# Kernel optimization log

Hardware: AMD Instinct MI355X
Metric: run time of the kernel (lower is better)

Reference implementation:

```python
import jax, jax.numpy as jnp
import numpy as np

EPS = 1e-08
LAMBDA_SIM = 1.0
LAMBDA_SPARSITY = 0.001
B, D, K = 8192, 4096, 64


def setup_inputs() -> dict:
    key = jax.random.key(0)
    k1, k2, k3, k4, k5 = jax.random.split(key, 5)
    labels = jax.random.randint(k1, (B,), 0, K)
    hard_class_probs = jax.nn.one_hot(labels, K, dtype=jnp.float32)  # [B,K] hard one-hot
    return {
        "hard_class_probs": hard_class_probs,
        "masked_activations_1b": jax.random.normal(k2, (B, D), dtype=jnp.float32),
        "masked_activations_8b": jax.random.normal(k3, (B, D), dtype=jnp.float32),
        "mask_1b": jax.random.uniform(k4, (B, D), dtype=jnp.float32),
        "mask_8b": jax.random.uniform(k5, (B, D), dtype=jnp.float32),
    }


def _classwise_pairwise_cossim(acts, hard_class_probs):
    # F.normalize(p=2, dim=-1, eps=EPS): x / max(||x||, eps)
    norms = jnp.sqrt(jnp.sum(acts * acts, axis=-1, keepdims=True))
    norm_acts = acts / jnp.maximum(norms, EPS)                      # [B,D]
    S = norm_acts @ norm_acts.T                                      # [B,B] gram of unit vectors
    diag = jnp.sum(norm_acts * norm_acts, axis=-1)                   # [B] (== diag(S))
    M = (hard_class_probs > 0.5).astype(acts.dtype)                  # [B,K] hard membership
    n = jnp.sum(M, axis=0)                                           # [K] class counts
    SM = S @ M                                                       # [B,K]
    mSm = jnp.sum(M * SM, axis=0)                                    # [K] sum_{i,j in class} S_ij
    sum_diag = M.T @ diag                                            # [K]
    pair_sum = 0.5 * (mSm - sum_diag)                                # sum over i<j pairs
    n_pairs = 0.5 * n * (n - 1.0)
    valid = n >= 2.0
    per_class_mean = jnp.where(valid, pair_sum / jnp.maximum(n_pairs, 1.0), 0.0)
    n_valid = jnp.sum(valid.astype(acts.dtype))
    return jnp.where(n_valid > 0, jnp.sum(per_class_mean) / jnp.maximum(n_valid, 1.0), 0.0)


def _binary_entropy(p):
    p = jnp.clip(p, EPS, 1.0 - EPS)
    return jnp.mean(-(p * jnp.log(p) + (1.0 - p) * jnp.log(1.0 - p)))


def _combined_loss(hard_class_probs, masked_activations, mask):
    sim_loss = -_classwise_pairwise_cossim(masked_activations, hard_class_probs)
    sparsity_loss = _binary_entropy(mask)
    total = LAMBDA_SIM * sim_loss + LAMBDA_SPARSITY * sparsity_loss
    return total, sim_loss, sparsity_loss


def reference(hard_class_probs, masked_activations_1b, masked_activations_8b, mask_1b, mask_8b):
    loss_1b, sim_1b, sp_1b = _combined_loss(hard_class_probs, masked_activations_1b, mask_1b)
    loss_8b, sim_8b, sp_8b = _combined_loss(hard_class_probs, masked_activations_8b, mask_8b)
    total_loss = loss_1b + loss_8b
    return (total_loss, sim_1b, sim_8b, sp_1b, sp_8b)
```

## Files before the change

kernel.cpp:

```cpp
#include <hip/hip_runtime.h>
#include <math.h>

#define B_ 8192
#define D_ 4096
#define K_ 64
#define EPSF 1e-8f
#define LN2F 0.69314718056f
#define ENT_GRID 2048
#define SPLITS 16

typedef float f32x4 __attribute__((ext_vector_type(4)));


__global__ void k_init(int* __restrict__ z) {
  if (threadIdx.x < 192) z[threadIdx.x] = 0;
}

__global__ void k_labels(const float* __restrict__ probs, int* __restrict__ labels,
                         int* __restrict__ counts, int* __restrict__ rowlist) {
  int row = blockIdx.x * 4 + (threadIdx.x >> 6);
  int lane = threadIdx.x & 63;
  float p = probs[(size_t)row * K_ + lane];
  unsigned long long m = __ballot(p > 0.5f);
  if (lane == 0) {
    int k = __ffsll(m) - 1;
    if (k >= 0) {
      labels[row] = k;
      int pos = atomicAdd(&counts[k], 1);
      rowlist[k * B_ + pos] = row;
    }
  }
}

__global__ __launch_bounds__(256) void k_classnorm(
    const float* __restrict__ a1, const float* __restrict__ a8,
    const int* __restrict__ counts, const int* __restrict__ rowlist,
    const int* __restrict__ labels, float* __restrict__ Cpart1, float* __restrict__ Cpart8,
    float* __restrict__ sd1, float* __restrict__ sd8) {
  int bid = blockIdx.x;
  const float* a = (bid < 256) ? a1 : a8;
  float* Cpart = (bid < 256) ? Cpart1 : Cpart8;
  float* sd = (bid < 256) ? sd1 : sd8;
  bid &= 255;
  int k = bid & 63;
  int blkSplit = bid >> 6;
  int wave = threadIdx.x >> 6;
  int lane = threadIdx.x & 63;
  int split = blkSplit * 4 + wave;
  int cnt = counts[k];
  int beg = (cnt * split) / SPLITS;
  int end = (cnt * (split + 1)) / SPLITS;
  const int* rl = rowlist + k * B_;

  f32x4 acc[16];
#pragma unroll
  for (int j = 0; j < 16; ++j) acc[j] = 0.f;

  for (int r = beg; r < end; ++r) {
    int row = rl[r];
    const f32x4* rp = (const f32x4*)(a + (size_t)row * D_);
    f32x4 v[16];
#pragma unroll
    for (int j = 0; j < 16; ++j) v[j] = rp[lane + 64 * j];
    float s = 0.f;
#pragma unroll
    for (int j = 0; j < 16; ++j)
      s += v[j].x * v[j].x + v[j].y * v[j].y + v[j].z * v[j].z + v[j].w * v[j].w;
#pragma unroll
    for (int o = 32; o > 0; o >>= 1) s += __shfl_xor(s, o);
    float w = 1.0f / fmaxf(sqrtf(s), EPSF);
#pragma unroll
    for (int j = 0; j < 16; ++j) acc[j] += w * v[j];
    if (lane == 0) atomicAdd(&sd[labels[row]], s * w * w);
  }

  float* cp = Cpart + ((size_t)split * K_ + k) * D_;
#pragma unroll
  for (int j = 0; j < 16; ++j) *(f32x4*)(cp + 4 * (lane + 64 * j)) = acc[j];
}

__global__ __launch_bounds__(256) void k_msm(const float* __restrict__ Cpart1,
                                             const float* __restrict__ Cpart8,
                                             float* __restrict__ msp1,
                                             float* __restrict__ msp8) {
  __shared__ float lds[4];
  int b = blockIdx.x;
  const float* Cpart = (b < 256) ? Cpart1 : Cpart8;
  float* msp = (b < 256) ? msp1 : msp8;
  b &= 255;
  int k = b >> 2;
  int q = b & 3;
  int t = threadIdx.x;
  int col = q * 1024 + 4 * t;
  f32x4 c = 0.f;
#pragma unroll
  for (int s = 0; s < SPLITS; ++s)
    c += *(const f32x4*)(Cpart + ((size_t)s * K_ + k) * D_ + col);
  float sq = c.x * c.x + c.y * c.y + c.z * c.z + c.w * c.w;
#pragma unroll
  for (int o = 32; o > 0; o >>= 1) sq += __shfl_down(sq, o);
  if ((t & 63) == 0) lds[t >> 6] = sq;
  __syncthreads();
  if (t == 0) msp[blockIdx.x & 255] = lds[0] + lds[1] + lds[2] + lds[3];
}

__device__ __forceinline__ float ent1(float p) {
  p = fminf(fmaxf(p, EPSF), 1.0f - EPSF);
  float q = 1.0f - p;
  float lp = __builtin_amdgcn_logf(p);
  float lq = __builtin_amdgcn_logf(fmaxf(q, 1e-38f));
  return -(p * lp + q * lq);
}

__device__ __forceinline__ float ent4(f32x4 v) {
  return ent1(v.x) + ent1(v.y) + ent1(v.z) + ent1(v.w);
}

__global__ __launch_bounds__(256) void k_entropy(const f32x4* __restrict__ m1,
                                                 const f32x4* __restrict__ m8,
                                                 double* __restrict__ entpart) {
  __shared__ float lds[8];
  const int CHUNK = (B_ * D_ / 4) / ENT_GRID;
  int base = blockIdx.x * CHUNK;
  int t = threadIdx.x;
  float s1 = 0.f, s8 = 0.f;
#pragma unroll
  for (int o = 0; o < 4; ++o) {
    f32x4 a[4], b[4];
#pragma unroll
    for (int j = 0; j < 4; ++j) {
      int idx = base + t + (o * 4 + j) * 256;
      a[j] = m1[idx];
      b[j] = m8[idx];
    }
#pragma unroll
    for (int j = 0; j < 4; ++j) {
      s1 += ent4(a[j]);
      s8 += ent4(b[j]);
    }
  }
#pragma unroll
  for (int o = 32; o > 0; o >>= 1) {
    s1 += __shfl_down(s1, o);
    s8 += __shfl_down(s8, o);
  }
  int wid = t >> 6;
  if ((t & 63) == 0) { lds[wid] = s1; lds[4 + wid] = s8; }
  __syncthreads();
  if (t == 0) {
    float t1 = lds[0] + lds[1] + lds[2] + lds[3];
    float t8 = lds[4] + lds[5] + lds[6] + lds[7];
    entpart[blockIdx.x]            = (double)(t1 * LN2F);
    entpart[ENT_GRID + blockIdx.x] = (double)(t8 * LN2F);
  }
}

__global__ void k_final(const double* __restrict__ entpart, const int* __restrict__ counts,
                        const float* __restrict__ sd1, const float* __restrict__ sd8,
                        const float* __restrict__ msp1, const float* __restrict__ msp8,
                        float* __restrict__ out) {
  __shared__ double dl[8];
  int t = threadIdx.x;
  double e1 = 0.0, e8 = 0.0;
  for (int i = t; i < ENT_GRID; i += 256) {
    e1 += entpart[i];
    e8 += entpart[ENT_GRID + i];
  }
#pragma unroll
  for (int o = 32; o > 0; o >>= 1) {
    e1 += __shfl_down(e1, o);
    e8 += __shfl_down(e8, o);
  }
  int wid = t >> 6;
  if ((t & 63) == 0) { dl[wid] = e1; dl[4 + wid] = e8; }
  __syncthreads();
  float pcm1 = 0.f, pcm8 = 0.f, valid = 0.f;
  if (t < K_) {
    float mSm1 = msp1[t * 4] + msp1[t * 4 + 1] + msp1[t * 4 + 2] + msp1[t * 4 + 3];
    float mSm8 = msp8[t * 4] + msp8[t * 4 + 1] + msp8[t * 4 + 2] + msp8[t * 4 + 3];
    float n = (float)counts[t];
    bool v = (n >= 2.0f);
    float np = fmaxf(0.5f * n * (n - 1.0f), 1.0f);
    valid = v ? 1.0f : 0.f;
    pcm1 = v ? 0.5f * (mSm1 - sd1[t]) / np : 0.f;
    pcm8 = v ? 0.5f * (mSm8 - sd8[t]) / np : 0.f;
  }
#pragma unroll
  for (int o = 32; o > 0; o >>= 1) {
    pcm1 += __shfl_down(pcm1, o);
    pcm8 += __shfl_down(pcm8, o);
    valid += __shfl_down(valid, o);
  }
  if (t == 0) {
    double etot1 = dl[0] + dl[1] + dl[2] + dl[3];
    double etot8 = dl[4] + dl[5] + dl[6] + dl[7];
    float sp1 = (float)(etot1 / (double)((long long)B_ * D_));
    float sp8 = (float)(etot8 / (double)((long long)B_ * D_));
    float cs1 = (valid > 0.f) ? pcm1 / fmaxf(valid, 1.0f) : 0.f;
    float cs8 = (valid > 0.f) ? pcm8 / fmaxf(valid, 1.0f) : 0.f;
    float sim1 = -cs1, sim8 = -cs8;
    out[0] = sim1 + sim8 + 0.001f * (sp1 + sp8);
    out[1] = sim1;
    out[2] = sim8;
    out[3] = sp1;
    out[4] = sp8;
  }
}


extern "C" void kernel_launch(void* const* d_in, const int* in_sizes, int n_in,
                              void* d_out, int out_size, void* d_ws, size_t ws_size,
                              hipStream_t stream) {
  const float* probs = (const float*)d_in[0];
  const float* a1 = (const float*)d_in[1];
  const float* a8 = (const float*)d_in[2];
  const float* m1 = (const float*)d_in[3];
  const float* m8 = (const float*)d_in[4];
  float* out = (float*)d_out;
  char* ws = (char*)d_ws;

  double* entpart = (double*)(ws + 0);
  int* labels = (int*)(ws + 32768);
  int* counts = (int*)(ws + 65536);
  float* sd1 = (float*)(ws + 65792);
  float* sd8 = (float*)(ws + 66048);
  float* msp1 = (float*)(ws + 66304);
  float* msp8 = (float*)(ws + 67328);
  int* rowlist = (int*)(ws + 69632);
  float* Cpart1 = (float*)(ws + 2166784);
  float* Cpart8 = (float*)(ws + 18944000);

  k_init<<<1, 256, 0, stream>>>(counts);
  k_labels<<<B_ / 4, 256, 0, stream>>>(probs, labels, counts, rowlist);
  k_classnorm<<<512, 256, 0, stream>>>(a1, a8, counts, rowlist, labels, Cpart1, Cpart8, sd1,
                                       sd8);
  k_entropy<<<ENT_GRID, 256, 0, stream>>>((const f32x4*)m1, (const f32x4*)m8, entpart);
  k_msm<<<512, 256, 0, stream>>>(Cpart1, Cpart8, msp1, msp8);
  k_final<<<1, 256, 0, stream>>>(entpart, counts, sd1, sd8, msp1, msp8, out);
}
```

Baseline: 183.6 us.

## Split each activation row across four waves with LDS norm reduction

The class-norm kernel now has one block per (class, split), and its four waves each cover a quarter of a row's columns instead of each wave handling whole rows. The squared norm is combined across waves through a double-buffered shared-memory array with a block barrier on every row. This cuts the per-wave register footprint from sixteen vector accumulators to four, quadruples the block count to fill more of the GPU, and drops the labels lookup for the atomic. The cost is a __syncthreads per row and a smaller per-wave memory footprint in flight.

```diff
diff --git a/kernel.cpp b/kernel.cpp
--- a/kernel.cpp
+++ b/kernel.cpp
@@ -35,48 +35,55 @@
 __global__ __launch_bounds__(256) void k_classnorm(
     const float* __restrict__ a1, const float* __restrict__ a8,
     const int* __restrict__ counts, const int* __restrict__ rowlist,
-    const int* __restrict__ labels, float* __restrict__ Cpart1, float* __restrict__ Cpart8,
-    float* __restrict__ sd1, float* __restrict__ sd8) {
+    float* __restrict__ Cpart1, float* __restrict__ Cpart8, float* __restrict__ sd1,
+    float* __restrict__ sd8) {
+  __shared__ float lred[2][4];
   int bid = blockIdx.x;
-  const float* a = (bid < 256) ? a1 : a8;
-  float* Cpart = (bid < 256) ? Cpart1 : Cpart8;
-  float* sd = (bid < 256) ? sd1 : sd8;
-  bid &= 255;
+  const int NBLK = K_ * SPLITS;
+  const float* a = (bid < NBLK) ? a1 : a8;
+  float* Cpart = (bid < NBLK) ? Cpart1 : Cpart8;
+  float* sd = (bid < NBLK) ? sd1 : sd8;
+  bid = (bid < NBLK) ? bid : bid - NBLK;
   int k = bid & 63;
-  int blkSplit = bid >> 6;
+  int split = bid >> 6;
   int wave = threadIdx.x >> 6;
   int lane = threadIdx.x & 63;
-  int split = blkSplit * 4 + wave;
   int cnt = counts[k];
   int beg = (cnt * split) / SPLITS;
   int end = (cnt * (split + 1)) / SPLITS;
   const int* rl = rowlist + k * B_;
 
-  f32x4 acc[16];
-#pragma unroll
-  for (int j = 0; j < 16; ++j) acc[j] = 0.f;
-
-  for (int r = beg; r < end; ++r) {
+  f32x4 acc0 = 0.f, acc1 = 0.f, acc2 = 0.f, acc3 = 0.f;
+  int par = 0;
+  for (int r = beg; r < end; ++r, par ^= 1) {
     int row = rl[r];
-    const f32x4* rp = (const f32x4*)(a + (size_t)row * D_);
-    f32x4 v[16];
-#pragma unroll
-    for (int j = 0; j < 16; ++j) v[j] = rp[lane + 64 * j];
-    float s = 0.f;
-#pragma unroll
-    for (int j = 0; j < 16; ++j)
-      s += v[j].x * v[j].x + v[j].y * v[j].y + v[j].z * v[j].z + v[j].w * v[j].w;
+    const f32x4* rp = (const f32x4*)(a + (size_t)row * D_) + (wave * 256 + lane);
+    f32x4 v0 = rp[0];
+    f32x4 v1 = rp[64];
+    f32x4 v2 = rp[128];
+    f32x4 v3 = rp[192];
+    float s = v0.x * v0.x + v0.y * v0.y + v0.z * v0.z + v0.w * v0.w;
+    s += v1.x * v1.x + v1.y * v1.y + v1.z * v1.z + v1.w * v1.w;
+    s += v2.x * v2.x + v2.y * v2.y + v2.z * v2.z + v2.w * v2.w;
+    s += v3.x * v3.x + v3.y * v3.y + v3.z * v3.z + v3.w * v3.w;
 #pragma unroll
     for (int o = 32; o > 0; o >>= 1) s += __shfl_xor(s, o);
-    float w = 1.0f / fmaxf(sqrtf(s), EPSF);
-#pragma unroll
-    for (int j = 0; j < 16; ++j) acc[j] += w * v[j];
-    if (lane == 0) atomicAdd(&sd[labels[row]], s * w * w);
-  }
-
-  float* cp = Cpart + ((size_t)split * K_ + k) * D_;
-#pragma unroll
-  for (int j = 0; j < 16; ++j) *(f32x4*)(cp + 4 * (lane + 64 * j)) = acc[j];
+    if (lane == 0) lred[par][wave] = s;
+    __syncthreads();
+    float stot = lred[par][0] + lred[par][1] + lred[par][2] + lred[par][3];
+    float w = 1.0f / fmaxf(sqrtf(stot), EPSF);
+    acc0 += w * v0;
+    acc1 += w * v1;
+    acc2 += w * v2;
+    acc3 += w * v3;
+    if (threadIdx.x == 0) atomicAdd(&sd[k], stot * w * w);
+  }
+
+  float* cp = Cpart + ((size_t)split * K_ + k) * D_ + wave * 1024;
+  *(f32x4*)(cp + 4 * lane) = acc0;
+  *(f32x4*)(cp + 4 * (64 + lane)) = acc1;
+  *(f32x4*)(cp + 4 * (128 + lane)) = acc2;
+  *(f32x4*)(cp + 4 * (192 + lane)) = acc3;
 }
 
 __global__ __launch_bounds__(256) void k_msm(const float* __restrict__ Cpart1,
@@ -232,8 +239,8 @@
 
   k_init<<<1, 256, 0, stream>>>(counts);
   k_labels<<<B_ / 4, 256, 0, stream>>>(probs, labels, counts, rowlist);
-  k_classnorm<<<512, 256, 0, stream>>>(a1, a8, counts, rowlist, labels, Cpart1, Cpart8, sd1,
-                                       sd8);
+  k_classnorm<<<2 * K_ * SPLITS, 256, 0, stream>>>(a1, a8, counts, rowlist, Cpart1, Cpart8,
+                                                   sd1, sd8);
   k_entropy<<<ENT_GRID, 256, 0, stream>>>((const f32x4*)m1, (const f32x4*)m8, entpart);
   k_msm<<<512, 256, 0, stream>>>(Cpart1, Cpart8, msp1, msp8);
   k_final<<<1, 256, 0, stream>>>(entpart, counts, sd1, sd8, msp1, msp8, out);
```

New measurement: 193.1 us. 5.1% more time.

## Fuse class-norm and entropy passes into a persistent work-stealing kernel

Applied to the files above, without the earlier changes.

Merges the class-sum and binary-entropy kernels into one persistent kernel whose waves take interleaved tasks from an atomic counter, so both memory-bound streams run at once and load balance across the GPU. Row loads in the class-sum path are double-buffered to overlap memory with compute. Splits per class double to 32, which needs a larger Cpart workspace and gives k_msm twice as many partials to reduce. The per-row sd atomic becomes one per-task atomic, and the labels array is dropped. The cost is a global atomic per task and higher register pressure from the two 16-vector buffers.

```diff
diff --git a/kernel.cpp b/kernel.cpp
--- a/kernel.cpp
+++ b/kernel.cpp
@@ -7,17 +7,17 @@
 #define EPSF 1e-8f
 #define LN2F 0.69314718056f
 #define ENT_GRID 2048
-#define SPLITS 16
+#define SPLITS 32
+#define GTASKS 4096
+#define TTASKS 8192
 
 typedef float f32x4 __attribute__((ext_vector_type(4)));
 
 
-__global__ void k_init(int* __restrict__ z) {
-  if (threadIdx.x < 192) z[threadIdx.x] = 0;
-}
-
-__global__ void k_labels(const float* __restrict__ probs, int* __restrict__ labels,
-                         int* __restrict__ counts, int* __restrict__ rowlist) {
+__global__ void k_init(int* __restrict__ z) { z[threadIdx.x] = 0; }
+
+__global__ void k_labels(const float* __restrict__ probs, int* __restrict__ counts,
+                         int* __restrict__ rowlist) {
   int row = blockIdx.x * 4 + (threadIdx.x >> 6);
   int lane = threadIdx.x & 63;
   float p = probs[(size_t)row * K_ + lane];
@@ -25,58 +25,100 @@
   if (lane == 0) {
     int k = __ffsll(m) - 1;
     if (k >= 0) {
-      labels[row] = k;
       int pos = atomicAdd(&counts[k], 1);
       rowlist[k * B_ + pos] = row;
     }
   }
 }
 
-__global__ __launch_bounds__(256) void k_classnorm(
+__device__ __forceinline__ float ent1(float p) {
+  p = fminf(fmaxf(p, EPSF), 1.0f - EPSF);
+  float q = 1.0f - p;
+  float lp = __builtin_amdgcn_logf(p);
+  float lq = __builtin_amdgcn_logf(fmaxf(q, 1e-38f));
+  return -(p * lp + q * lq);
+}
+
+__device__ __forceinline__ float ent4(f32x4 v) {
+  return ent1(v.x) + ent1(v.y) + ent1(v.z) + ent1(v.w);
+}
+
+#define MLOADROW(V, ROW)                                                        \
+  {                                                                             \
+    const f32x4* rp_ = (const f32x4*)(a + (size_t)(ROW)*D_) + lane;             \
+    _Pragma("unroll") for (int j = 0; j < 16; ++j) V[j] = rp_[64 * j];          \
+  }
+
+#define MCONSUME(V)                                                             \
+  {                                                                             \
+    float s_ = 0.f;                                                             \
+    _Pragma("unroll") for (int j = 0; j < 16; ++j) s_ +=                        \
+        V[j].x * V[j].x + V[j].y * V[j].y + V[j].z * V[j].z + V[j].w * V[j].w;  \
+    _Pragma("unroll") for (int o = 32; o > 0; o >>= 1) s_ += __shfl_xor(s_, o); \
+    float w_ = 1.0f / fmaxf(sqrtf(s_), EPSF);                                   \
+    _Pragma("unroll") for (int j = 0; j < 16; ++j) acc[j] += w_ * V[j];         \
+    sdacc += s_ * w_ * w_;                                                      \
+  }
+
+__global__ __launch_bounds__(256) void k_mega(
     const float* __restrict__ a1, const float* __restrict__ a8,
+    const f32x4* __restrict__ m1, const f32x4* __restrict__ m8,
     const int* __restrict__ counts, const int* __restrict__ rowlist,
-    const int* __restrict__ labels, float* __restrict__ Cpart1, float* __restrict__ Cpart8,
-    float* __restrict__ sd1, float* __restrict__ sd8) {
-  int bid = blockIdx.x;
-  const float* a = (bid < 256) ? a1 : a8;
-  float* Cpart = (bid < 256) ? Cpart1 : Cpart8;
-  float* sd = (bid < 256) ? sd1 : sd8;
-  bid &= 255;
-  int k = bid & 63;
-  int blkSplit = bid >> 6;
-  int wave = threadIdx.x >> 6;
+    float* __restrict__ Cpart1, float* __restrict__ Cpart8, float* __restrict__ sd1,
+    float* __restrict__ sd8, double* __restrict__ entpart, int* __restrict__ ctr) {
   int lane = threadIdx.x & 63;
-  int split = blkSplit * 4 + wave;
-  int cnt = counts[k];
-  int beg = (cnt * split) / SPLITS;
-  int end = (cnt * (split + 1)) / SPLITS;
-  const int* rl = rowlist + k * B_;
-
-  f32x4 acc[16];
-#pragma unroll
-  for (int j = 0; j < 16; ++j) acc[j] = 0.f;
-
-  for (int r = beg; r < end; ++r) {
-    int row = rl[r];
-    const f32x4* rp = (const f32x4*)(a + (size_t)row * D_);
-    f32x4 v[16];
-#pragma unroll
-    for (int j = 0; j < 16; ++j) v[j] = rp[lane + 64 * j];
-    float s = 0.f;
-#pragma unroll
-    for (int j = 0; j < 16; ++j)
-      s += v[j].x * v[j].x + v[j].y * v[j].y + v[j].z * v[j].z + v[j].w * v[j].w;
-#pragma unroll
-    for (int o = 32; o > 0; o >>= 1) s += __shfl_xor(s, o);
-    float w = 1.0f / fmaxf(sqrtf(s), EPSF);
-#pragma unroll
-    for (int j = 0; j < 16; ++j) acc[j] += w * v[j];
-    if (lane == 0) atomicAdd(&sd[labels[row]], s * w * w);
-  }
-
-  float* cp = Cpart + ((size_t)split * K_ + k) * D_;
-#pragma unroll
-  for (int j = 0; j < 16; ++j) *(f32x4*)(cp + 4 * (lane + 64 * j)) = acc[j];
+  for (;;) {
+    int task = 0;
+    if (lane == 0) task = atomicAdd(ctr, 1);
+    task = __shfl(task, 0);
+    if (task >= TTASKS) break;
+    int id = task >> 1;
+    if (task & 1) {
+      const f32x4* base = ((id >> 11) ? m8 : m1) + (size_t)(id & 2047) * 4096;
+      double* ep = entpart + ((id >> 11) ? ENT_GRID : 0);
+      float s = 0.f;
+      for (int o = 0; o < 8; ++o) {
+        f32x4 v[8];
+#pragma unroll
+        for (int j = 0; j < 8; ++j) v[j] = base[lane + (o * 8 + j) * 64];
+#pragma unroll
+        for (int j = 0; j < 8; ++j) s += ent4(v[j]);
+      }
+#pragma unroll
+      for (int o = 32; o > 0; o >>= 1) s += __shfl_xor(s, o);
+      if (lane == 0) ep[id & 2047] = (double)(s * LN2F);
+    } else {
+      const float* a = (id >> 11) ? a8 : a1;
+      float* Cpart = (id >> 11) ? Cpart8 : Cpart1;
+      float* sd = (id >> 11) ? sd8 : sd1;
+      int k = id & 63;
+      int split = (id & 2047) >> 6;
+      int cnt = counts[k];
+      int beg = (cnt * split) / SPLITS;
+      int end = (cnt * (split + 1)) / SPLITS;
+      const int* rl = rowlist + k * B_;
+      f32x4 acc[16];
+#pragma unroll
+      for (int j = 0; j < 16; ++j) acc[j] = 0.f;
+      float sdacc = 0.f;
+      f32x4 va[16], vb[16];
+      int r = beg;
+      if (end > beg) {
+        MLOADROW(va, rl[r]);
+        for (; r + 2 <= end; r += 2) {
+          MLOADROW(vb, rl[r + 1]);
+          MCONSUME(va);
+          if (r + 2 < end) MLOADROW(va, rl[r + 2]);
+          MCONSUME(vb);
+        }
+        if (r < end) MCONSUME(va);
+      }
+      float* cp = Cpart + ((size_t)split * K_ + k) * D_;
+#pragma unroll
+      for (int j = 0; j < 16; ++j) *(f32x4*)(cp + 4 * (lane + 64 * j)) = acc[j];
+      if (lane == 0 && sdacc != 0.f) atomicAdd(&sd[k], sdacc);
+    }
+  }
 }
 
 __global__ __launch_bounds__(256) void k_msm(const float* __restrict__ Cpart1,
@@ -93,7 +135,6 @@
   int t = threadIdx.x;
   int col = q * 1024 + 4 * t;
   f32x4 c = 0.f;
-#pragma unroll
   for (int s = 0; s < SPLITS; ++s)
     c += *(const f32x4*)(Cpart + ((size_t)s * K_ + k) * D_ + col);
   float sq = c.x * c.x + c.y * c.y + c.z * c.z + c.w * c.w;
@@ -102,57 +143,6 @@
   if ((t & 63) == 0) lds[t >> 6] = sq;
   __syncthreads();
   if (t == 0) msp[blockIdx.x & 255] = lds[0] + lds[1] + lds[2] + lds[3];
-}
-
-__device__ __forceinline__ float ent1(float p) {
-  p = fminf(fmaxf(p, EPSF), 1.0f - EPSF);
-  float q = 1.0f - p;
-  float lp = __builtin_amdgcn_logf(p);
-  float lq = __builtin_amdgcn_logf(fmaxf(q, 1e-38f));
-  return -(p * lp + q * lq);
-}
-
-__device__ __forceinline__ float ent4(f32x4 v) {
-  return ent1(v.x) + ent1(v.y) + ent1(v.z) + ent1(v.w);
-}
-
-__global__ __launch_bounds__(256) void k_entropy(const f32x4* __restrict__ m1,
-                                                 const f32x4* __restrict__ m8,
-                                                 double* __restrict__ entpart) {
-  __shared__ float lds[8];
-  const int CHUNK = (B_ * D_ / 4) / ENT_GRID;
-  int base = blockIdx.x * CHUNK;
-  int t = threadIdx.x;
-  float s1 = 0.f, s8 = 0.f;
-#pragma unroll
-  for (int o = 0; o < 4; ++o) {
-    f32x4 a[4], b[4];
-#pragma unroll
-    for (int j = 0; j < 4; ++j) {
-      int idx = base + t + (o * 4 + j) * 256;
-      a[j] = m1[idx];
-      b[j] = m8[idx];
-    }
-#pragma unroll
-    for (int j = 0; j < 4; ++j) {
-      s1 += ent4(a[j]);
-      s8 += ent4(b[j]);
-    }
-  }
-#pragma unroll
-  for (int o = 32; o > 0; o >>= 1) {
-    s1 += __shfl_down(s1, o);
-    s8 += __shfl_down(s8, o);
-  }
-  int wid = t >> 6;
-  if ((t & 63) == 0) { lds[wid] = s1; lds[4 + wid] = s8; }
-  __syncthreads();
-  if (t == 0) {
-    float t1 = lds[0] + lds[1] + lds[2] + lds[3];
-    float t8 = lds[4] + lds[5] + lds[6] + lds[7];
-    entpart[blockIdx.x]            = (double)(t1 * LN2F);
-    entpart[ENT_GRID + blockIdx.x] = (double)(t8 * LN2F);
-  }
 }
 
 __global__ void k_final(const double* __restrict__ entpart, const int* __restrict__ counts,
@@ -220,21 +210,20 @@
   char* ws = (char*)d_ws;
 
   double* entpart = (double*)(ws + 0);
-  int* labels = (int*)(ws + 32768);
-  int* counts = (int*)(ws + 65536);
-  float* sd1 = (float*)(ws + 65792);
-  float* sd8 = (float*)(ws + 66048);
-  float* msp1 = (float*)(ws + 66304);
-  float* msp8 = (float*)(ws + 67328);
-  int* rowlist = (int*)(ws + 69632);
-  float* Cpart1 = (float*)(ws + 2166784);
-  float* Cpart8 = (float*)(ws + 18944000);
+  int* counts = (int*)(ws + 32768);
+  float* sd1 = (float*)(ws + 33024);
+  float* sd8 = (float*)(ws + 33280);
+  int* ctr = (int*)(ws + 33536);
+  float* msp1 = (float*)(ws + 33792);
+  float* msp8 = (float*)(ws + 34816);
+  int* rowlist = (int*)(ws + 65536);
+  float* Cpart1 = (float*)(ws + 2162688);
+  float* Cpart8 = (float*)(ws + 35717120);
 
   k_init<<<1, 256, 0, stream>>>(counts);
-  k_labels<<<B_ / 4, 256, 0, stream>>>(probs, labels, counts, rowlist);
-  k_classnorm<<<512, 256, 0, stream>>>(a1, a8, counts, rowlist, labels, Cpart1, Cpart8, sd1,
-                                       sd8);
-  k_entropy<<<ENT_GRID, 256, 0, stream>>>((const f32x4*)m1, (const f32x4*)m8, entpart);
+  k_labels<<<B_ / 4, 256, 0, stream>>>(probs, counts, rowlist);
+  k_mega<<<768, 256, 0, stream>>>(a1, a8, (const f32x4*)m1, (const f32x4*)m8, counts,
+                                  rowlist, Cpart1, Cpart8, sd1, sd8, entpart, ctr);
   k_msm<<<512, 256, 0, stream>>>(Cpart1, Cpart8, msp1, msp8);
   k_final<<<1, 256, 0, stream>>>(entpart, counts, sd1, sd8, msp1, msp8, out);
 }
```

New measurement: 224.0 us. 22.0% more time.
